# Performance work log

Measured on AMD Instinct MI355X. Metric: run time of the kernel, lower is better.

Reference implementation:

```python
import jax, jax.numpy as jnp
import numpy as np

V, E, H, L, HID, T, B = 50257, 512, 8, 8, 1365, 1024, 2
HD = E // H
EPS = 1e-5


def setup_inputs() -> dict:
    key = jax.random.key(0)
    ks = jax.random.split(key, 9)
    s = 0.02
    def nrm(k, shape):
        return jax.random.normal(k, shape, jnp.float32) * s
    return {
        "idx": jax.random.randint(ks[0], (B, T), 0, V),
        "W_emb": nrm(ks[1], (V, E)),          # tied tok_emb / lm head
        "pos_emb": nrm(ks[2], (T, E)),
        "ln1_s": jnp.ones((L, E)), "ln1_b": jnp.zeros((L, E)),
        "qkv_w": nrm(ks[3], (L, E, 3 * E)),
        "proj_w": nrm(ks[4], (L, E, E)),
        "ln2_s": jnp.ones((L, E)), "ln2_b": jnp.zeros((L, E)),
        "gate_w": nrm(ks[5], (L, E, HID)),
        "up_w": nrm(ks[6], (L, E, HID)),
        "down_w": nrm(ks[7], (L, HID, E)),
        "lnf_s": jnp.ones((E,)), "lnf_b": jnp.zeros((E,)),
    }


def _ln(x, s, b):
    m = x.mean(-1, keepdims=True)
    v = ((x - m) ** 2).mean(-1, keepdims=True)
    return (x - m) * jax.lax.rsqrt(v + EPS) * s + b


def _forward(idx, W_emb, pos_emb, ln1_s, ln1_b, qkv_w, proj_w,
             ln2_s, ln2_b, gate_w, up_w, down_w, lnf_s, lnf_b):
    x = W_emb[idx] + pos_emb[None, :, :]  # [B,T,E]
    pos = jnp.arange(T)
    # faithful to source: ALiBi bias uses |i-j|, added before causal mask
    dist = jnp.abs(pos[None, :] - pos[:, None]).astype(jnp.float32)  # [T,T]
    slopes = (1.0 / 2.0 ** (8.0 * jnp.arange(1, H + 1, dtype=jnp.float32) / H))
    alibi = slopes[:, None, None] * dist[None]  # [H,T,T]
    causal = jnp.tril(jnp.ones((T, T), bool))
    scale = 1.0 / np.sqrt(HD)

    def block(x, p):
        l1s, l1b, qkvw, pw, l2s, l2b, gw, uw, dw = p
        h = _ln(x, l1s, l1b)
        qkv = h @ qkvw  # [B,T,3E]
        q, k, v = jnp.split(qkv, 3, axis=-1)
        q = q.reshape(B, T, H, HD).transpose(0, 2, 1, 3)
        k = k.reshape(B, T, H, HD).transpose(0, 2, 1, 3)
        v = v.reshape(B, T, H, HD).transpose(0, 2, 1, 3)
        att = jnp.einsum('bhqd,bhkd->bhqk', q, k) * scale + alibi[None]
        att = jnp.where(causal, att, -jnp.inf)
        att = jax.nn.softmax(att, axis=-1)
        o = jnp.einsum('bhqk,bhkd->bhqd', att, v)
        o = o.transpose(0, 2, 1, 3).reshape(B, T, E)
        x = x + o @ pw
        h = _ln(x, l2s, l2b)
        g = h @ gw
        x = x + (g * jax.nn.sigmoid(g) * (h @ uw)) @ dw  # SwiGLU
        return x, None

    x, _ = jax.lax.scan(block, x, (ln1_s, ln1_b, qkv_w, proj_w,
                                   ln2_s, ln2_b, gate_w, up_w, down_w))
    x = _ln(x, lnf_s, lnf_b)
    return x @ W_emb.T  # tied head -> [B,T,V]


def reference(idx, W_emb, pos_emb, ln1_s, ln1_b, qkv_w, proj_w,
              ln2_s, ln2_b, gate_w, up_w, down_w, lnf_s, lnf_b):
    return _forward(idx, W_emb, pos_emb, ln1_s, ln1_b, qkv_w, proj_w,
                    ln2_s, ln2_b, gate_w, up_w, down_w, lnf_s, lnf_b)
```

## Files before the change

kernel.cpp:

```cpp
#include <hip/hip_runtime.h>
#include <hip/hip_bf16.h>
#include <math.h>

#define V_SZ 50257
#define V_PAD 50304
#define E_SZ 512
#define H_N 8
#define L_N 8
#define HID_SZ 1365
#define HID_PAD 1408
#define T_SZ 1024
#define B_SZ 2
#define HD_SZ 64
#define ROWS (B_SZ * T_SZ)

typedef short bf16x8 __attribute__((ext_vector_type(8)));
typedef float f32x4 __attribute__((ext_vector_type(4)));
typedef float f32x16 __attribute__((ext_vector_type(16)));

__global__ __launch_bounds__(128) void embed_kernel(
    const int* __restrict__ idx, const float* __restrict__ W,
    const float* __restrict__ P, float* __restrict__ x,
    float* __restrict__ stats) {
  const int bt = blockIdx.x;
  const int t = bt & (T_SZ - 1);
  const int id = idx[bt];
  const int e = threadIdx.x * 4;
  float4 w = *(const float4*)(W + (size_t)id * E_SZ + e);
  float4 p = *(const float4*)(P + (size_t)t * E_SZ + e);
  float4 r;
  r.x = w.x + p.x; r.y = w.y + p.y; r.z = w.z + p.z; r.w = w.w + p.w;
  *(float4*)(x + (size_t)bt * E_SZ + e) = r;
  float s = r.x + r.y + r.z + r.w;
  float q = r.x * r.x + r.y * r.y + r.z * r.z + r.w * r.w;
#pragma unroll
  for (int o = 32; o; o >>= 1) { s += __shfl_xor(s, o); q += __shfl_xor(q, o); }
  __shared__ float sr[4];
  if ((threadIdx.x & 63) == 0) {
    sr[(threadIdx.x >> 6) * 2] = s;
    sr[(threadIdx.x >> 6) * 2 + 1] = q;
  }
  __syncthreads();
  if (threadIdx.x < 16) {
    float a = (threadIdx.x == 0) ? sr[0] + sr[2] : 0.f;
    float b2 = (threadIdx.x == 0) ? sr[1] + sr[3] : 0.f;
    float* st = stats + (size_t)bt * 32 + threadIdx.x * 2;
    st[0] = a; st[1] = b2;
  }
}

__global__ __launch_bounds__(256) void ln_from_stats(
    const float* __restrict__ x, const float* __restrict__ stats,
    const float* __restrict__ gamma, const float* __restrict__ beta,
    __hip_bfloat16* __restrict__ out) {
  const int row = blockIdx.x;
  const int tid = threadIdx.x;
  const float* sp = stats + (size_t)row * 32;
  float sum = 0.f, ssq = 0.f;
#pragma unroll
  for (int i = 0; i < 8; ++i) {
    float4 v = ((const float4*)sp)[i];
    sum += v.x + v.z; ssq += v.y + v.w;
  }
  const float mean = sum * (1.f / 512.f);
  const float var = ssq * (1.f / 512.f) - mean * mean;
  const float rstd = rsqrtf(var + 1e-5f);
  const float2 v = *(const float2*)(x + (size_t)row * E_SZ + tid * 2);
  const float2 sv = *(const float2*)(gamma + tid * 2);
  const float2 bv = *(const float2*)(beta + tid * 2);
  __hip_bfloat162 ov;
  ov.x = __float2bfloat16((v.x - mean) * rstd * sv.x + bv.x);
  ov.y = __float2bfloat16((v.y - mean) * rstd * sv.y + bv.y);
  *(__hip_bfloat162*)(out + (size_t)row * E_SZ + tid * 2) = ov;
}

__global__ __launch_bounds__(256) void convert_wemb(
    const float* __restrict__ W, __hip_bfloat16* __restrict__ Wb) {
  const int tid = blockIdx.x * 256 + threadIdx.x;
  const int row = tid >> 6;
  const int c = (tid & 63) * 8;
  union { __hip_bfloat16 h[8]; int4 v; } u;
  if (row < V_SZ) {
    const float* p = W + (size_t)row * E_SZ + c;
#pragma unroll
    for (int j = 0; j < 8; ++j) u.h[j] = __float2bfloat16(p[j]);
  } else {
#pragma unroll
    for (int j = 0; j < 8; ++j) u.h[j] = __float2bfloat16(0.f);
  }
  *(int4*)(Wb + (size_t)row * E_SZ + c) = u.v;
}

__global__ __launch_bounds__(256) void transp_convert(
    const float* __restrict__ in, __hip_bfloat16* __restrict__ out,
    int K, int N, int Kpad, int Npad) {
  __shared__ float tile[32][33];
  const int l = blockIdx.z;
  in  += (size_t)l * K * N;
  out += (size_t)l * Npad * Kpad;
  const int tx = threadIdx.x & 31, ty = threadIdx.x >> 5;
  const int n0 = blockIdx.x * 32, k0 = blockIdx.y * 32;
#pragma unroll
  for (int i = 0; i < 4; ++i) {
    const int k = k0 + ty + i * 8, n = n0 + tx;
    tile[ty + i * 8][tx] = (k < K && n < N) ? in[(size_t)k * N + n] : 0.f;
  }
  __syncthreads();
#pragma unroll
  for (int i = 0; i < 4; ++i) {
    const int n = n0 + ty + i * 8, kk = k0 + tx;
    out[(size_t)n * Kpad + kk] = __float2bfloat16(tile[tx][ty + i * 8]);
  }
}

__global__ __launch_bounds__(256) void gu_prep(
    const float* __restrict__ gate, const float* __restrict__ up,
    __hip_bfloat16* __restrict__ outw) {
  __shared__ float tile[32][33];
  const int l = blockIdx.z;
  const int c0 = blockIdx.x * 32, k0 = blockIdx.y * 32;
  const int tx = threadIdx.x & 31, ty = threadIdx.x >> 5;
#pragma unroll
  for (int role = 0; role < 2; ++role) {
    const float* src = (role ? up : gate) + (size_t)l * E_SZ * HID_SZ;
#pragma unroll
    for (int i = 0; i < 4; ++i) {
      const int k = k0 + ty + i * 8, c = c0 + tx;
      tile[ty + i * 8][tx] = (c < HID_SZ) ? src[(size_t)k * HID_SZ + c] : 0.f;
    }
    __syncthreads();
#pragma unroll
    for (int i = 0; i < 4; ++i) {
      const int c = c0 + ty + i * 8, kk = k0 + tx;
      const int n = ((c >> 4) << 5) | (role << 4) | (c & 15);
      outw[((size_t)l * 2816 + n) * E_SZ + kk] = __float2bfloat16(tile[tx][ty + i * 8]);
    }
    __syncthreads();
  }
}

template <int EPI>
__global__ __launch_bounds__(256) void gemm64ln(
    const float* __restrict__ X, const __hip_bfloat16* __restrict__ B,
    void* __restrict__ Cv, const float* __restrict__ stats,
    const float* __restrict__ gamma, const float* __restrict__ beta,
    int N, int K) {
  __shared__ char lds[16384];
  __shared__ float gb[1024];
  const int tid = threadIdx.x, lane = tid & 63, w = tid >> 6;
  const int wr = w >> 1, wc = w & 1;
  const int m0 = blockIdx.y * 64, n0 = blockIdx.x * 64;
  const size_t SB = (size_t)K * 2;
  char* As = lds;
  char* Bs = lds + 8192;
  const char* Bb = (const char*)B + (size_t)n0 * SB;
  f32x4 acc[2][2] = {};
  const int lrow = lane >> 3;
  const int schunk = ((lane & 7) ^ lrow) * 16;
  const int kb = (lane >> 4) * 16;

  for (int i = tid; i < 512; i += 256) { gb[i] = gamma[i]; gb[512 + i] = beta[i]; }

  const int arow = tid >> 2, acol = (tid & 3) * 16;
  const int achunk0 = acol >> 3;
  const int akey = arow & 7;
  float mean, rstd;
  {
    const float* sp = stats + (size_t)(m0 + arow) * 32;
    float sum = 0.f, ssq = 0.f;
#pragma unroll
    for (int i = 0; i < 8; ++i) {
      float4 v = ((const float4*)sp)[i];
      sum += v.x + v.z; ssq += v.y + v.w;
    }
    mean = sum * (1.f / 512.f);
    const float var = ssq * (1.f / 512.f) - mean * mean;
    rstd = rsqrtf(var + 1e-5f);
  }
  const float* Xrow = X + (size_t)(m0 + arow) * K;
  __syncthreads();

  for (int k0 = 0; k0 < K; k0 += 64) {
#pragma unroll
    for (int i = 0; i < 2; ++i) {
      const int row = w * 8 + 32 * i + lrow;
      const char* gbp = Bb + (size_t)row * SB + k0 * 2 + schunk;
      __builtin_amdgcn_global_load_lds(
          (const __attribute__((address_space(1))) unsigned int*)gbp,
          (__attribute__((address_space(3))) unsigned int*)(Bs + w * 1024 + i * 4096),
          16, 0, 0);
    }
    {
      float xf[16];
      const float* xs = Xrow + k0 + acol;
      *(float4*)&xf[0]  = ((const float4*)xs)[0];
      *(float4*)&xf[4]  = ((const float4*)xs)[1];
      *(float4*)&xf[8]  = ((const float4*)xs)[2];
      *(float4*)&xf[12] = ((const float4*)xs)[3];
      union { __hip_bfloat16 h[16]; int4 v[2]; } pk;
#pragma unroll
      for (int jj = 0; jj < 16; ++jj) {
        const int col = k0 + acol + jj;
        pk.h[jj] = __float2bfloat16((xf[jj] - mean) * rstd * gb[col] + gb[512 + col]);
      }
      *(int4*)(As + arow * 128 + (((achunk0 + 0) ^ akey) * 16)) = pk.v[0];
      *(int4*)(As + arow * 128 + (((achunk0 + 1) ^ akey) * 16)) = pk.v[1];
    }
    __syncthreads();
    bf16x8 a[2][2], bb[2][2];
#pragma unroll
    for (int i = 0; i < 2; ++i) {
      const int ra = wr * 32 + i * 16 + (lane & 15);
      const int rb = wc * 32 + i * 16 + (lane & 15);
#pragma unroll
      for (int ks = 0; ks < 2; ++ks) {
        a[i][ks]  = *(const bf16x8*)(As + ra * 128 + ((ks * 64 + kb) ^ ((ra & 7) << 4)));
        bb[i][ks] = *(const bf16x8*)(Bs + rb * 128 + ((ks * 64 + kb) ^ ((rb & 7) << 4)));
      }
    }
#pragma unroll
    for (int ks = 0; ks < 2; ++ks)
#pragma unroll
      for (int i = 0; i < 2; ++i)
#pragma unroll
        for (int j = 0; j < 2; ++j)
          acc[i][j] = __builtin_amdgcn_mfma_f32_16x16x32_bf16(a[i][ks], bb[j][ks], acc[i][j], 0, 0, 0);
    __syncthreads();
  }

  const int cr = (lane >> 4) * 4, ccol = lane & 15;
  if (EPI == 3) {
    __hip_bfloat16* G = (__hip_bfloat16*)Cv;
    const int cg = (n0 >> 1) + wc * 16 + ccol;
#pragma unroll
    for (int i = 0; i < 2; ++i) {
#pragma unroll
      for (int rr = 0; rr < 4; ++rr) {
        const int m = m0 + wr * 32 + i * 16 + cr + rr;
        const float gv = acc[i][0][rr];
        const float uv = acc[i][1][rr];
        const float val = gv / (1.f + __expf(-gv)) * uv;
        G[(size_t)m * HID_PAD + cg] = __float2bfloat16(val);
      }
    }
  } else {
    __hip_bfloat16* O = (__hip_bfloat16*)Cv;
#pragma unroll
    for (int i = 0; i < 2; ++i)
#pragma unroll
      for (int j = 0; j < 2; ++j) {
        const int n = n0 + wc * 32 + j * 16 + ccol;
#pragma unroll
        for (int rr = 0; rr < 4; ++rr) {
          const int m = m0 + wr * 32 + i * 16 + cr + rr;
          O[(size_t)m * N + n] = __float2bfloat16(acc[i][j][rr]);
        }
      }
  }
}

__global__ __launch_bounds__(256) void gemm64(
    const __hip_bfloat16* __restrict__ A, const __hip_bfloat16* __restrict__ B,
    float* __restrict__ C, const float* __restrict__ R,
    float* __restrict__ stats, int N, int K) {
  __shared__ char lds[16384];
  const int tid = threadIdx.x, lane = tid & 63, w = tid >> 6;
  const int wr = w >> 1, wc = w & 1;
  const int m0 = blockIdx.y * 64, n0 = blockIdx.x * 64;
  const size_t SA = (size_t)K * 2;
  char* As = lds;
  char* Bs = lds + 8192;
  const char* Ab = (const char*)A + (size_t)m0 * SA;
  const char* Bb = (const char*)B + (size_t)n0 * SA;
  f32x4 acc[2][2] = {};
  const int lrow = lane >> 3;
  const int schunk = ((lane & 7) ^ lrow) * 16;
  const int kb = (lane >> 4) * 16;

  for (int k0 = 0; k0 < K; k0 += 64) {
#pragma unroll
    for (int i = 0; i < 2; ++i) {
      const int row = w * 8 + 32 * i + lrow;
      const char* ga = Ab + (size_t)row * SA + k0 * 2 + schunk;
      __builtin_amdgcn_global_load_lds(
          (const __attribute__((address_space(1))) unsigned int*)ga,
          (__attribute__((address_space(3))) unsigned int*)(As + w * 1024 + i * 4096),
          16, 0, 0);
      const char* gbp = Bb + (size_t)row * SA + k0 * 2 + schunk;
      __builtin_amdgcn_global_load_lds(
          (const __attribute__((address_space(1))) unsigned int*)gbp,
          (__attribute__((address_space(3))) unsigned int*)(Bs + w * 1024 + i * 4096),
          16, 0, 0);
    }
    __syncthreads();
    bf16x8 a[2][2], bb[2][2];
#pragma unroll
    for (int i = 0; i < 2; ++i) {
      const int ra = wr * 32 + i * 16 + (lane & 15);
      const int rb = wc * 32 + i * 16 + (lane & 15);
#pragma unroll
      for (int ks = 0; ks < 2; ++ks) {
        a[i][ks]  = *(const bf16x8*)(As + ra * 128 + ((ks * 64 + kb) ^ ((ra & 7) << 4)));
        bb[i][ks] = *(const bf16x8*)(Bs + rb * 128 + ((ks * 64 + kb) ^ ((rb & 7) << 4)));
      }
    }
#pragma unroll
    for (int ks = 0; ks < 2; ++ks)
#pragma unroll
      for (int i = 0; i < 2; ++i)
#pragma unroll
        for (int j = 0; j < 2; ++j)
          acc[i][j] = __builtin_amdgcn_mfma_f32_16x16x32_bf16(a[i][ks], bb[j][ks], acc[i][j], 0, 0, 0);
    __syncthreads();
  }

  const int cr = (lane >> 4) * 4, ccol = lane & 15;
  float vv[2][2][4];
#pragma unroll
  for (int i = 0; i < 2; ++i)
#pragma unroll
    for (int j = 0; j < 2; ++j) {
      const int n = n0 + wc * 32 + j * 16 + ccol;
#pragma unroll
      for (int rr = 0; rr < 4; ++rr) {
        const int m = m0 + wr * 32 + i * 16 + cr + rr;
        const float v = acc[i][j][rr] + R[(size_t)m * N + n];
        vv[i][j][rr] = v;
        C[(size_t)m * N + n] = v;
      }
    }
  const int slice = blockIdx.x * 2 + wc;
#pragma unroll
  for (int i = 0; i < 2; ++i) {
#pragma unroll
    for (int rr = 0; rr < 4; ++rr) {
      float s = vv[i][0][rr] + vv[i][1][rr];
      float q = vv[i][0][rr] * vv[i][0][rr] + vv[i][1][rr] * vv[i][1][rr];
#pragma unroll
      for (int o = 1; o < 16; o <<= 1) { s += __shfl_xor(s, o); q += __shfl_xor(q, o); }
      if ((lane & 15) == 0) {
        const int m = m0 + wr * 32 + i * 16 + cr + rr;
        float* st = stats + (size_t)m * 32 + slice * 2;
        st[0] = s; st[1] = q;
      }
    }
  }
}

__global__ __launch_bounds__(256) void head_gemm(
    const __hip_bfloat16* __restrict__ A, const __hip_bfloat16* __restrict__ B,
    float* __restrict__ C, int N, int K) {
  __shared__ char lds[49152];
  const int tid = threadIdx.x;
  const int lane = tid & 63, w = tid >> 6;
  const int wr = w >> 1, wc = w & 1;
  const int nwg = gridDim.x * gridDim.y;
  const int id = blockIdx.y * gridDim.x + blockIdx.x;
  const int work = (id & 7) * (nwg >> 3) + (id >> 3);
  const int bx = work >> 4, by = work & 15;
  const int m0 = by * 128, n0 = bx * 128;
  const size_t SA = (size_t)K * 2;

  f32x4 acc[4][4] = {};
  const char* Ab = (const char*)A + (size_t)m0 * SA;
  const char* Bb = (const char*)B + (size_t)n0 * SA;

  const int srow = tid >> 2, schnk = tid & 3;

  auto STAGE = [&](int buf, int t) {
    char* As = lds + buf * 16384;
    char* Bs = As + 8192;
    const int k0b = t * 64;
#pragma unroll
    for (int i = 0; i < 2; ++i) {
      const int r = srow + i * 64;
      const int gc = (schnk ^ (r & 3)) * 16;
      const char* ga = Ab + (size_t)r * SA + k0b + gc;
      __builtin_amdgcn_global_load_lds(
          (const __attribute__((address_space(1))) unsigned int*)ga,
          (__attribute__((address_space(3))) unsigned int*)(As + i * 4096 + tid * 16),
          16, 0, 0);
      const char* gbp = Bb + (size_t)r * SA + k0b + gc;
      __builtin_amdgcn_global_load_lds(
          (const __attribute__((address_space(1))) unsigned int*)gbp,
          (__attribute__((address_space(3))) unsigned int*)(Bs + i * 4096 + tid * 16),
          16, 0, 0);
    }
  };

  const int kb = lane >> 4;
  STAGE(0, 0);
  STAGE(1, 1);
#pragma unroll
  for (int t = 0; t < 16; ++t) {
    if (t + 2 < 16) STAGE((t + 2) % 3, t + 2);
    if (t <= 13)      asm volatile("s_waitcnt vmcnt(8)" ::: "memory");
    else if (t == 14) asm volatile("s_waitcnt vmcnt(4)" ::: "memory");
    else              asm volatile("s_waitcnt vmcnt(0)" ::: "memory");
    __builtin_amdgcn_s_barrier();
    asm volatile("" ::: "memory");
    const char* As = lds + (t % 3) * 16384;
    const char* Bs = As + 8192;
    bf16x8 a[4], b[4];
#pragma unroll
    for (int i = 0; i < 4; ++i) {
      const int ra = wr * 64 + i * 16 + (lane & 15);
      const int rb = wc * 64 + i * 16 + (lane & 15);
      a[i] = *(const bf16x8*)(As + ra * 64 + ((kb ^ (ra & 3)) * 16));
      b[i] = *(const bf16x8*)(Bs + rb * 64 + ((kb ^ (rb & 3)) * 16));
    }
    __builtin_amdgcn_s_setprio(1);
#pragma unroll
    for (int i = 0; i < 4; ++i)
#pragma unroll
      for (int j = 0; j < 4; ++j)
        acc[i][j] = __builtin_amdgcn_mfma_f32_16x16x32_bf16(a[i], b[j], acc[i][j], 0, 0, 0);
    __builtin_amdgcn_s_setprio(0);
    asm volatile("" ::: "memory");
    __builtin_amdgcn_s_barrier();
    asm volatile("" ::: "memory");
  }

  const int cr = (lane >> 4) * 4, ccol = lane & 15;
#pragma unroll
  for (int i = 0; i < 4; ++i) {
#pragma unroll
    for (int j = 0; j < 4; ++j) {
      const int n = n0 + wc * 64 + j * 16 + ccol;
      if (n >= N) continue;
#pragma unroll
      for (int rr = 0; rr < 4; ++rr) {
        const int m = m0 + wr * 64 + i * 16 + cr + rr;
        C[(size_t)m * N + n] = acc[i][j][rr];
      }
    }
  }
}

__global__ __launch_bounds__(256, 1) void attn_mfma_kernel(
    const __hip_bfloat16* __restrict__ qkv, __hip_bfloat16* __restrict__ o) {
  const int bid = blockIdx.x;
  const int qb = bid & 15;
  const int h = (bid >> 4) & 7;
  const int b = bid >> 7;
  const int tid = threadIdx.x;
  const int w = tid >> 6, lane = tid & 63;
  const int g = w >> 1;
  const int wq = w & 1;
  const int l31 = lane & 31, hi = lane >> 5;
  const int q0w = qb * 64 + 32 * wq;
  const float slope = exp2f(-(float)(h + 1));
  const int rowstride = 3 * E_SZ;
  const int nch = qb + 1;
  const int niter = (nch + 1) >> 1;

  __shared__ char lds[32768];
  char* Kb = lds + g * 16384;
  char* Vb = Kb + 8192;

  bf16x8 qf[4];
  {
    const __hip_bfloat16* qrow = qkv + (size_t)(b * T_SZ + q0w + l31) * rowstride + h * HD_SZ;
#pragma unroll
    for (int dblk = 0; dblk < 4; ++dblk)
      qf[dblk] = *(const bf16x8*)(qrow + dblk * 16 + hi * 8);
  }

  f32x16 oacc[2][2] = {};
  float m[2] = {-INFINITY, -INFINITY}, lsum[2] = {0.f, 0.f};

  int4 kreg[4];
  int4 va[2], vb[2];
  const int ltid = tid & 127;
  const int jK = ltid >> 1, halfK = ltid & 1;
  const int jqV = ltid >> 2, qtV = ltid & 3;
  const int j0V = jqV * 2, d0V = qtV * 16;

  auto ISSUE = [&](int c) {
    const __hip_bfloat16* srcK = qkv + (size_t)(b * T_SZ + c * 64 + jK) * rowstride + E_SZ + h * HD_SZ + halfK * 32;
    kreg[0] = ((const int4*)srcK)[0]; kreg[1] = ((const int4*)srcK)[1];
    kreg[2] = ((const int4*)srcK)[2]; kreg[3] = ((const int4*)srcK)[3];
    const __hip_bfloat16* srcV = qkv + (size_t)(b * T_SZ + c * 64 + j0V) * rowstride + 2 * E_SZ + h * HD_SZ + d0V;
    va[0] = ((const int4*)srcV)[0]; va[1] = ((const int4*)srcV)[1];
    vb[0] = ((const int4*)(srcV + rowstride))[0]; vb[1] = ((const int4*)(srcV + rowstride))[1];
  };
  auto WRITE = [&]() {
#pragma unroll
    for (int u2 = 0; u2 < 4; ++u2) {
      const int d0 = halfK * 32 + u2 * 8;
      *(int4*)(Kb + jK * 128 + ((2 * d0) ^ ((jK & 7) << 4))) = kreg[u2];
    }
    union { int4 v[2]; unsigned short us[16]; } ua, ub;
    ua.v[0] = va[0]; ua.v[1] = va[1];
    ub.v[0] = vb[0]; ub.v[1] = vb[1];
#pragma unroll
    for (int e = 0; e < 16; ++e) {
      const int d = d0V + e;
      const unsigned wv = (unsigned)ua.us[e] | ((unsigned)ub.us[e] << 16);
      *(unsigned*)(Vb + d * 128 + ((2 * j0V) ^ ((d & 7) << 4))) = wv;
    }
  };

  if (g < nch) ISSUE(g);
  for (int it = 0; it < niter; ++it) {
    const int c = 2 * it + g;
    const bool act = c < nch;
    if (act) WRITE();
    __syncthreads();
    if (c + 2 < nch) ISSUE(c + 2);
    if (act) {
#pragma unroll
      for (int s = 0; s < 2; ++s) {
        const int j0 = c * 64 + 32 * s;
        if (j0 <= q0w + 31) {
          const int st = s;
          f32x16 sacc = {};
          const int jrow = 32 * s + l31;
          __builtin_amdgcn_s_setprio(1);
#pragma unroll
          for (int dblk = 0; dblk < 4; ++dblk) {
            bf16x8 kf = *(const bf16x8*)(Kb + jrow * 128 + ((dblk * 32 + hi * 16) ^ ((jrow & 7) << 4)));
            sacc = __builtin_amdgcn_mfma_f32_32x32x16_bf16(kf, qf[dblk], sacc, 0, 0, 0);
          }
          __builtin_amdgcn_s_setprio(0);
          const int qg = q0w + l31;
          float p[16];
          float tmax = -1e30f;
#pragma unroll
          for (int r = 0; r < 16; ++r) {
            const int jg = j0 + (r & 3) + 8 * (r >> 2) + 4 * hi;
            const float sv = (jg > qg) ? -1e9f : (sacc[r] * 0.125f + slope * (float)(qg - jg));
            p[r] = sv;
            tmax = fmaxf(tmax, sv);
          }
          tmax = fmaxf(tmax, __shfl_xor(tmax, 32));
          if (!__all(tmax <= m[st] + 8.f)) {
            const float mnew = fmaxf(m[st], tmax);
            const float corr = __expf(m[st] - mnew);
            lsum[st] *= corr;
#pragma unroll
            for (int dt = 0; dt < 2; ++dt)
#pragma unroll
              for (int r = 0; r < 16; ++r) oacc[st][dt][r] *= corr;
            m[st] = mnew;
          }
          float tsum = 0.f;
#pragma unroll
          for (int r = 0; r < 16; ++r) {
            p[r] = __expf(p[r] - m[st]);
            tsum += p[r];
          }
          tsum += __shfl_xor(tsum, 32);
          lsum[st] += tsum;
          unsigned wds[8];
#pragma unroll
          for (int k = 0; k < 8; ++k) {
            union { __hip_bfloat16 hh[2]; unsigned u; } pk_;
            pk_.hh[0] = __float2bfloat16(p[2 * k]);
            pk_.hh[1] = __float2bfloat16(p[2 * k + 1]);
            wds[k] = pk_.u;
          }
          bf16x8 pfrag[2];
#pragma unroll
          for (int jb = 0; jb < 2; ++jb) {
            const unsigned w0 = wds[4 * jb + 0], w1 = wds[4 * jb + 1];
            const unsigned w2 = wds[4 * jb + 2], w3 = wds[4 * jb + 3];
            const unsigned x2 = (unsigned)__shfl_xor((int)w2, 32);
            const unsigned x3 = (unsigned)__shfl_xor((int)w3, 32);
            const unsigned x0 = (unsigned)__shfl_xor((int)w0, 32);
            const unsigned x1 = (unsigned)__shfl_xor((int)w1, 32);
            union { unsigned u[4]; bf16x8 v; } pf;
            pf.u[0] = hi ? x2 : w0;
            pf.u[1] = hi ? x3 : w1;
            pf.u[2] = hi ? w2 : x0;
            pf.u[3] = hi ? w3 : x1;
            pfrag[jb] = pf.v;
          }
          __builtin_amdgcn_s_setprio(1);
#pragma unroll
          for (int dt = 0; dt < 2; ++dt) {
            const int row = dt * 32 + l31;
#pragma unroll
            for (int jb = 0; jb < 2; ++jb) {
              bf16x8 vt = *(const bf16x8*)(Vb + row * 128 + ((s * 64 + jb * 32 + hi * 16) ^ ((row & 7) << 4)));
              oacc[st][dt] = __builtin_amdgcn_mfma_f32_32x32x16_bf16(vt, pfrag[jb], oacc[st][dt], 0, 0, 0);
            }
          }
          __builtin_amdgcn_s_setprio(0);
        }
      }
    }
    __syncthreads();
  }

  float mW, lW;
  float Ow[2][16];
  if (g < nch) {
    const float mm = fmaxf(m[0], m[1]);
    const float a = __expf(m[0] - mm), b2 = __expf(m[1] - mm);
    mW = mm;
    lW = lsum[0] * a + lsum[1] * b2;
#pragma unroll
    for (int dt = 0; dt < 2; ++dt)
#pragma unroll
      for (int r = 0; r < 16; ++r)
        Ow[dt][r] = oacc[0][dt][r] * a + oacc[1][dt][r] * b2;
  } else {
    mW = -INFINITY; lW = 0.f;
#pragma unroll
    for (int dt = 0; dt < 2; ++dt)
#pragma unroll
      for (int r = 0; r < 16; ++r) Ow[dt][r] = 0.f;
  }

  float* Obuf = (float*)lds + wq * 2048;
  float* mlb  = (float*)lds + 4096 + wq * 64;
  __syncthreads();
  if (g == 1) {
#pragma unroll
    for (int dt = 0; dt < 2; ++dt)
#pragma unroll
      for (int r = 0; r < 16; ++r)
        Obuf[lane * 32 + dt * 16 + r] = Ow[dt][r];
    if (hi == 0) { mlb[l31 * 2] = mW; mlb[l31 * 2 + 1] = lW; }
  }
  __syncthreads();
  if (g == 0) {
    const float m1 = mlb[l31 * 2], l1 = mlb[l31 * 2 + 1];
    const float mmF = fmaxf(mW, m1);
    const float wA = __expf(mW - mmF), wB = __expf(m1 - mmF);
    const float inv = 1.f / (lW * wA + l1 * wB);
    __hip_bfloat16* orow = o + (size_t)(b * T_SZ + q0w + l31) * E_SZ + h * HD_SZ;
#pragma unroll
    for (int dt = 0; dt < 2; ++dt) {
#pragma unroll
      for (int gq = 0; gq < 4; ++gq) {
        union { __hip_bfloat16 hh[4]; short4 v; } ov;
#pragma unroll
        for (int e = 0; e < 4; ++e) {
          const int r = 4 * gq + e;
          const float o1 = Obuf[lane * 32 + dt * 16 + r];
          ov.hh[e] = __float2bfloat16((Ow[dt][r] * wA + o1 * wB) * inv);
        }
        *(short4*)(orow + dt * 32 + 4 * hi + 8 * gq) = ov.v;
      }
    }
  }
}

extern "C" void kernel_launch(void* const* d_in, const int* in_sizes, int n_in,
                              void* d_out, int out_size, void* d_ws, size_t ws_size,
                              hipStream_t stream) {
  const int* idx      = (const int*)d_in[0];
  const float* W_emb  = (const float*)d_in[1];
  const float* pos    = (const float*)d_in[2];
  const float* ln1_s  = (const float*)d_in[3];
  const float* ln1_b  = (const float*)d_in[4];
  const float* qkv_w  = (const float*)d_in[5];
  const float* proj_w = (const float*)d_in[6];
  const float* ln2_s  = (const float*)d_in[7];
  const float* ln2_b  = (const float*)d_in[8];
  const float* gate_w = (const float*)d_in[9];
  const float* up_w   = (const float*)d_in[10];
  const float* down_w = (const float*)d_in[11];
  const float* lnf_s  = (const float*)d_in[12];
  const float* lnf_b  = (const float*)d_in[13];
  float* out = (float*)d_out;

  char* p = (char*)d_ws;
  auto alloc = [&](size_t bytes) { char* q = p; p += (bytes + 255) & ~255ULL; return q; };
  float* x      = (float*)alloc((size_t)ROWS * E_SZ * 4);
  float* statsA = (float*)alloc((size_t)ROWS * 32 * 4);
  float* statsB = (float*)alloc((size_t)ROWS * 32 * 4);
  __hip_bfloat16* qkv_bf = (__hip_bfloat16*)alloc((size_t)ROWS * 3 * E_SZ * 2);
  __hip_bfloat16* h_bf  = (__hip_bfloat16*)alloc((size_t)ROWS * E_SZ * 2);
  __hip_bfloat16* o_bf  = (__hip_bfloat16*)alloc((size_t)ROWS * E_SZ * 2);
  __hip_bfloat16* g_bf  = (__hip_bfloat16*)alloc((size_t)ROWS * HID_PAD * 2);
  __hip_bfloat16* Wb    = (__hip_bfloat16*)alloc((size_t)V_PAD * E_SZ * 2);
  __hip_bfloat16* qkvwb = (__hip_bfloat16*)alloc((size_t)L_N * 3 * E_SZ * E_SZ * 2);
  __hip_bfloat16* projwb= (__hip_bfloat16*)alloc((size_t)L_N * E_SZ * E_SZ * 2);
  __hip_bfloat16* guwb  = (__hip_bfloat16*)alloc((size_t)L_N * 2816 * E_SZ * 2);
  __hip_bfloat16* downwb= (__hip_bfloat16*)alloc((size_t)L_N * E_SZ * HID_PAD * 2);

  convert_wemb<<<(V_PAD * E_SZ / 8 + 255) / 256, 256, 0, stream>>>(W_emb, Wb);
  transp_convert<<<dim3(3 * E_SZ / 32, E_SZ / 32, L_N), 256, 0, stream>>>(
      qkv_w, qkvwb, E_SZ, 3 * E_SZ, E_SZ, 3 * E_SZ);
  transp_convert<<<dim3(E_SZ / 32, E_SZ / 32, L_N), 256, 0, stream>>>(
      proj_w, projwb, E_SZ, E_SZ, E_SZ, E_SZ);
  gu_prep<<<dim3(HID_PAD / 32, E_SZ / 32, L_N), 256, 0, stream>>>(gate_w, up_w, guwb);
  transp_convert<<<dim3(E_SZ / 32, HID_PAD / 32, L_N), 256, 0, stream>>>(
      down_w, downwb, HID_SZ, E_SZ, HID_PAD, E_SZ);

  embed_kernel<<<ROWS, 128, 0, stream>>>(idx, W_emb, pos, x, statsA);

  for (int l = 0; l < L_N; ++l) {
    gemm64ln<1><<<dim3(3 * E_SZ / 64, ROWS / 64), 256, 0, stream>>>(
        x, qkvwb + (size_t)l * 3 * E_SZ * E_SZ, qkv_bf, statsA,
        ln1_s + l * E_SZ, ln1_b + l * E_SZ, 3 * E_SZ, E_SZ);
    attn_mfma_kernel<<<B_SZ * H_N * (T_SZ / 64), 256, 0, stream>>>(qkv_bf, o_bf);
    gemm64<<<dim3(E_SZ / 64, ROWS / 64), 256, 0, stream>>>(
        o_bf, projwb + (size_t)l * E_SZ * E_SZ, x, x, statsB, E_SZ, E_SZ);
    gemm64ln<3><<<dim3(2816 / 64, ROWS / 64), 256, 0, stream>>>(
        x, guwb + (size_t)l * 2816 * E_SZ, g_bf, statsB,
        ln2_s + l * E_SZ, ln2_b + l * E_SZ, 2816, E_SZ);
    gemm64<<<dim3(E_SZ / 64, ROWS / 64), 256, 0, stream>>>(
        g_bf, downwb + (size_t)l * E_SZ * HID_PAD, x, x, statsA, E_SZ, HID_PAD);
  }

  ln_from_stats<<<ROWS, 256, 0, stream>>>(x, statsA, lnf_s, lnf_b, h_bf);
  head_gemm<<<dim3(V_PAD / 128, 16), 256, 0, stream>>>(h_bf, Wb, out, V_SZ, E_SZ);
}
```

Before: 1.138 ms.

## Triple-buffer gemm64 LDS tiles with async global_load_lds prefetch

Restructures the gemm64 K-loop into a three-stage LDS ring, so tiles two steps ahead are prefetched with global_load_lds while the current tile is consumed. Partial vmcnt waits replace full syncthreads, letting loads overlap MFMA work. It also raises wave priority around the MFMA block. LDS use triples to 48KB per block, which may reduce occupancy, and the hand-written vmcnt counts depend on each thread issuing exactly four loads per stage.

```diff
diff --git a/kernel.cpp b/kernel.cpp
--- a/kernel.cpp
+++ b/kernel.cpp
@@ -263,13 +263,11 @@
     const __hip_bfloat16* __restrict__ A, const __hip_bfloat16* __restrict__ B,
     float* __restrict__ C, const float* __restrict__ R,
     float* __restrict__ stats, int N, int K) {
-  __shared__ char lds[16384];
+  __shared__ char lds[49152];
   const int tid = threadIdx.x, lane = tid & 63, w = tid >> 6;
   const int wr = w >> 1, wc = w & 1;
   const int m0 = blockIdx.y * 64, n0 = blockIdx.x * 64;
   const size_t SA = (size_t)K * 2;
-  char* As = lds;
-  char* Bs = lds + 8192;
   const char* Ab = (const char*)A + (size_t)m0 * SA;
   const char* Bb = (const char*)B + (size_t)n0 * SA;
   f32x4 acc[2][2] = {};
@@ -277,22 +275,42 @@
   const int schunk = ((lane & 7) ^ lrow) * 16;
   const int kb = (lane >> 4) * 16;
 
-  for (int k0 = 0; k0 < K; k0 += 64) {
+  auto STAGE = [&](int buf, int t) {
+    char* As = lds + buf * 16384;
+    char* Bs = As + 8192;
+    const int k0b = t * 128;
 #pragma unroll
     for (int i = 0; i < 2; ++i) {
       const int row = w * 8 + 32 * i + lrow;
-      const char* ga = Ab + (size_t)row * SA + k0 * 2 + schunk;
+      const char* ga = Ab + (size_t)row * SA + k0b + schunk;
       __builtin_amdgcn_global_load_lds(
           (const __attribute__((address_space(1))) unsigned int*)ga,
           (__attribute__((address_space(3))) unsigned int*)(As + w * 1024 + i * 4096),
           16, 0, 0);
-      const char* gbp = Bb + (size_t)row * SA + k0 * 2 + schunk;
+      const char* gbp = Bb + (size_t)row * SA + k0b + schunk;
       __builtin_amdgcn_global_load_lds(
           (const __attribute__((address_space(1))) unsigned int*)gbp,
           (__attribute__((address_space(3))) unsigned int*)(Bs + w * 1024 + i * 4096),
           16, 0, 0);
     }
-    __syncthreads();
+  };
+
+  const int NT = K >> 6;
+  STAGE(0, 0);
+  if (NT > 1) STAGE(1, 1);
+  for (int t = 0; t < NT; ++t) {
+    if (t + 2 < NT) {
+      STAGE((t + 2) % 3, t + 2);
+      asm volatile("s_waitcnt vmcnt(8)" ::: "memory");
+    } else if (t + 1 < NT) {
+      asm volatile("s_waitcnt vmcnt(4)" ::: "memory");
+    } else {
+      asm volatile("s_waitcnt vmcnt(0)" ::: "memory");
+    }
+    __builtin_amdgcn_s_barrier();
+    asm volatile("" ::: "memory");
+    const char* As = lds + (t % 3) * 16384;
+    const char* Bs = As + 8192;
     bf16x8 a[2][2], bb[2][2];
 #pragma unroll
     for (int i = 0; i < 2; ++i) {
@@ -304,6 +322,7 @@
         bb[i][ks] = *(const bf16x8*)(Bs + rb * 128 + ((ks * 64 + kb) ^ ((rb & 7) << 4)));
       }
     }
+    __builtin_amdgcn_s_setprio(1);
 #pragma unroll
     for (int ks = 0; ks < 2; ++ks)
 #pragma unroll
@@ -311,7 +330,10 @@
 #pragma unroll
         for (int j = 0; j < 2; ++j)
           acc[i][j] = __builtin_amdgcn_mfma_f32_16x16x32_bf16(a[i][ks], bb[j][ks], acc[i][j], 0, 0, 0);
-    __syncthreads();
+    __builtin_amdgcn_s_setprio(0);
+    asm volatile("" ::: "memory");
+    __builtin_amdgcn_s_barrier();
+    asm volatile("" ::: "memory");
   }
 
   const int cr = (lane >> 4) * 4, ccol = lane & 15;
```

After: 1.070 ms. 6.0% less time.
